# Kernel tuning notes

Hardware: AMD Instinct MI355X
Metric: run time of the kernel (lower is better)

The kernel has to match this reference:

```python
import jax, jax.numpy as jnp
import numpy as np

B, T, C = 4, 2048, 1024
WIN = 16


def setup_inputs() -> dict:
    key = jax.random.key(0)
    ks = jax.random.split(key, 5)
    s = 1.0 / np.sqrt(C)
    return {
        "x": jax.random.normal(ks[0], (B, T, C), dtype=jnp.float32),
        "Wq": jax.random.normal(ks[1], (C, C), dtype=jnp.float32) * s,
        "bq": jnp.zeros((C,), jnp.float32),
        "Wk": jax.random.normal(ks[2], (C, C), dtype=jnp.float32) * s,
        "bk": jnp.zeros((C,), jnp.float32),
        "Wv": jax.random.normal(ks[3], (C, C), dtype=jnp.float32) * s,
        "bv": jnp.zeros((C,), jnp.float32),
        "Wo": jax.random.normal(ks[4], (C, C), dtype=jnp.float32) * s,
        "bo": jnp.zeros((C,), jnp.float32),
        "window": WIN,
    }


def reference(x, Wq, bq, Wk, bk, Wv, bv, Wo, bo, window):
    Bn, Tn, Cn = x.shape
    half = window // 2
    W = 2 * half + 1  # keys per query (window [t-half, t+half])
    q = x @ Wq.T + bq
    k = x @ Wk.T + bk
    v = x @ Wv.T + bv
    offs = jnp.arange(-half, half + 1)              # [W]
    tpos = jnp.arange(Tn)                            # [T]
    idx = tpos[:, None] + offs[None, :]              # [T, W]
    valid = (idx >= 0) & (idx < Tn)                  # [T, W]
    idx_c = jnp.clip(idx, 0, Tn - 1)
    k_win = k[:, idx_c, :]                           # [B, T, W, C]
    v_win = v[:, idx_c, :]                           # [B, T, W, C]
    scale = 1.0 / jnp.sqrt(jnp.asarray(Cn, x.dtype))
    scores = jnp.einsum('btc,btwc->btw', q, k_win) * scale
    scores = jnp.where(valid[None, :, :], scores, jnp.finfo(x.dtype).min)
    attn = jax.nn.softmax(scores, axis=-1)           # [B, T, W]
    ctx = jnp.einsum('btw,btwc->btc', attn, v_win)   # [B, T, C]
    return ctx @ Wo.T + bo
```

## Files before the change

kernel.cpp:

```cpp
#include <hip/hip_runtime.h>
#include <cstdint>
#include <cstddef>

#define B_ 4
#define T_ 2048
#define C_ 1024
#define M_ (B_ * T_)
#define QK_STRIDE 2048
#define NT 32

typedef unsigned short u16;
typedef _Float16 half8 __attribute__((ext_vector_type(8)));
typedef float f32x16 __attribute__((ext_vector_type(16)));
typedef unsigned short ushort8v __attribute__((ext_vector_type(8)));

__device__ __forceinline__ ushort4 cvt4(float4 v) {
    ushort4 o;
    _Float16 a = (_Float16)v.x; o.x = __builtin_bit_cast(unsigned short, a);
    _Float16 b = (_Float16)v.y; o.y = __builtin_bit_cast(unsigned short, b);
    _Float16 c = (_Float16)v.z; o.z = __builtin_bit_cast(unsigned short, c);
    _Float16 d = (_Float16)v.w; o.w = __builtin_bit_cast(unsigned short, d);
    return o;
}


__global__ void prologue2(const float* __restrict__ x,
                          const float* __restrict__ Wq, const float* __restrict__ Wk,
                          const float* __restrict__ Wv, const float* __restrict__ Wo,
                          const float* __restrict__ bq, const float* __restrict__ bk,
                          const float* __restrict__ bv,
                          u16* __restrict__ xf, u16* __restrict__ wfq,
                          u16* __restrict__ wfo, float* __restrict__ bcat) {
    const int blk = blockIdx.x;
    const int tid = threadIdx.x;
    if (blk >= 3072) {
        int i = (blk - 3072) * 256 + tid;
        const float* src = (i < 1024) ? bq : (i < 2048) ? bk : bv;
        bcat[i] = src[i & 1023];
        return;
    }
    __shared__ ushort8v g16[512];
    const float* src;
    u16* dst;
    size_t chunk_base;
    int kg;
    if (blk < 2048) {
        const int mt = blk >> 3; kg = blk & 7;
        src = x + (size_t)mt * 32 * C_;
        dst = xf; chunk_base = (size_t)mt * 64;
    } else {
        const int w = blk - 2048;
        const int mat = w >> 8, nt = (w >> 3) & 31; kg = w & 7;
        src = ((mat == 0) ? Wq : (mat == 1) ? Wk : (mat == 2) ? Wv : Wo)
              + (size_t)nt * 32 * C_;
        if (mat < 3) { dst = wfq; chunk_base = (size_t)(mat * 32 + nt) * 64; }
        else         { dst = wfo; chunk_base = (size_t)nt * 64; }
    }
    const int r = tid >> 3, gc = (tid & 7) * 2;
    const float4* s4 = (const float4*)(src + (size_t)r * C_ + kg * 128 + (tid & 7) * 16);
    float4 f0 = s4[0], f1 = s4[1], f2 = s4[2], f3 = s4[3];
    ushort4 h0 = cvt4(f0), h1 = cvt4(f1), h2 = cvt4(f2), h3 = cvt4(f3);
    ushort8v ga, gb;
    ga[0]=h0.x; ga[1]=h0.y; ga[2]=h0.z; ga[3]=h0.w;
    ga[4]=h1.x; ga[5]=h1.y; ga[6]=h1.z; ga[7]=h1.w;
    gb[0]=h2.x; gb[1]=h2.y; gb[2]=h2.z; gb[3]=h2.w;
    gb[4]=h3.x; gb[5]=h3.y; gb[6]=h3.z; gb[7]=h3.w;
    g16[r * 16 + ((gc    ) ^ (r & 15))] = ga;
    g16[r * 16 + ((gc + 1) ^ (r & 15))] = gb;
    __syncthreads();
    const int lane = tid & 63, rr = lane & 31, hi = lane >> 5;
#pragma unroll
    for (int r2 = 0; r2 < 2; ++r2) {
        const int ksl = r2 * 4 + (tid >> 6);
        const int g = ksl * 2 + hi;
        ushort8v v = g16[rr * 16 + (g ^ (rr & 15))];
        *(ushort8v*)(dst + ((chunk_base + kg * 8 + ksl) * 64 + lane) * 8) = v;
    }
}

#define AS1_ __attribute__((address_space(1)))
#define AS3_ __attribute__((address_space(3)))

__device__ __forceinline__ void gload16(const u16* g, u16* l) {
    __builtin_amdgcn_global_load_lds((AS1_ void*)g, (AS3_ void*)l, 16, 0, 0);
}

#define MFMA_ __builtin_amdgcn_mfma_f32_32x32x16_f16
#define LD8_(p) (*(const half8*)(p))

#define STAGE(NB, KT) { const size_t ko = (size_t)(KT) * 1024;            \
    gload16(gA0 + ko, (NB) + lA0); gload16(gA1 + ko, (NB) + lA1);         \
    gload16(gA2 + ko, (NB) + lA2); gload16(gA3 + ko, (NB) + lA3);         \
    gload16(gB0 + ko, (NB) + lB0); gload16(gB1 + ko, (NB) + lB1); }

#define TILE(CB, NB, KT, DOSTG, VW)                                        \
  {                                                                        \
    half8 a0 = *(const half8*)((CB) + oA);                                 \
    half8 a1 = *(const half8*)((CB) + oA + 1024);                          \
    half8 a2 = *(const half8*)((CB) + oA + 2048);                          \
    half8 a3 = *(const half8*)((CB) + oA + 3072);                          \
    half8 b0v = *(const half8*)((CB) + oB);                                \
    half8 b1v = *(const half8*)((CB) + oB + 1024);                         \
    if (DOSTG) STAGE(NB, (KT) + 2);                                        \
    __builtin_amdgcn_s_setprio(1);                                         \
    acc00 = MFMA_(a0, b0v, acc00, 0, 0, 0);                                \
    acc01 = MFMA_(a0, b1v, acc01, 0, 0, 0);                                \
    acc10 = MFMA_(a1, b0v, acc10, 0, 0, 0);                                \
    acc11 = MFMA_(a1, b1v, acc11, 0, 0, 0);                                \
    acc20 = MFMA_(a2, b0v, acc20, 0, 0, 0);                                \
    acc21 = MFMA_(a2, b1v, acc21, 0, 0, 0);                                \
    acc30 = MFMA_(a3, b0v, acc30, 0, 0, 0);                                \
    acc31 = MFMA_(a3, b1v, acc31, 0, 0, 0);                                \
    __builtin_amdgcn_s_setprio(0);                                         \
    a0 = *(const half8*)((CB) + oA + 512);                                 \
    a1 = *(const half8*)((CB) + oA + 1536);                                \
    a2 = *(const half8*)((CB) + oA + 2560);                                \
    a3 = *(const half8*)((CB) + oA + 3584);                                \
    b0v = *(const half8*)((CB) + oB + 512);                                \
    b1v = *(const half8*)((CB) + oB + 1536);                               \
    __builtin_amdgcn_s_setprio(1);                                         \
    acc00 = MFMA_(a0, b0v, acc00, 0, 0, 0);                                \
    acc01 = MFMA_(a0, b1v, acc01, 0, 0, 0);                                \
    acc10 = MFMA_(a1, b0v, acc10, 0, 0, 0);                                \
    acc11 = MFMA_(a1, b1v, acc11, 0, 0, 0);                                \
    acc20 = MFMA_(a2, b0v, acc20, 0, 0, 0);                                \
    acc21 = MFMA_(a2, b1v, acc21, 0, 0, 0);                                \
    acc30 = MFMA_(a3, b0v, acc30, 0, 0, 0);                                \
    acc31 = MFMA_(a3, b1v, acc31, 0, 0, 0);                                \
    __builtin_amdgcn_s_setprio(0);                                         \
    if ((VW) == 6)      asm volatile("s_waitcnt vmcnt(6) lgkmcnt(0)" ::: "memory"); \
    else if ((VW) == 0) asm volatile("s_waitcnt vmcnt(0) lgkmcnt(0)" ::: "memory"); \
    else                asm volatile("s_waitcnt lgkmcnt(0)" ::: "memory"); \
    asm volatile("s_barrier" ::: "memory");                                \
  }

__global__ __launch_bounds__(256, 2) void gemm_p2(
    const u16* __restrict__ Afrag, const u16* __restrict__ Bfrag,
    const float* __restrict__ bias, u16* __restrict__ qkh,
    u16* __restrict__ vf)
{
    __shared__ u16 lds[3][12288];
    const int tid  = threadIdx.x;
    const int lane = tid & 63;
    const int wave = tid >> 6;
    const int wm   = wave >> 1;
    const int wn   = wave & 1;
    const int la8  = lane * 8;

    const int nb  = gridDim.x * gridDim.y;
    int bid = blockIdx.y * gridDim.x + blockIdx.x;
    bid = (bid & 7) * (nb >> 3) + (bid >> 3);
    const int bx = bid % gridDim.x;
    const int by = bid / gridDim.x;

    const u16* gA0 = Afrag + ((size_t)(by*8 + ((wave    )>>1))*64 + ((wave    )&1))*512 + la8;
    const u16* gA1 = Afrag + ((size_t)(by*8 + ((wave+ 4 )>>1))*64 + ((wave+ 4 )&1))*512 + la8;
    const u16* gA2 = Afrag + ((size_t)(by*8 + ((wave+ 8 )>>1))*64 + ((wave+ 8 )&1))*512 + la8;
    const u16* gA3 = Afrag + ((size_t)(by*8 + ((wave+12 )>>1))*64 + ((wave+12 )&1))*512 + la8;
    const u16* gB0 = Bfrag + ((size_t)(bx*4 + ((wave    )>>1))*64 + ((wave    )&1))*512 + la8;
    const u16* gB1 = Bfrag + ((size_t)(bx*4 + ((wave+ 4 )>>1))*64 + ((wave+ 4 )&1))*512 + la8;
    const int lA0 = (wave     ) * 512;
    const int lA1 = (wave +  4) * 512;
    const int lA2 = (wave +  8) * 512;
    const int lA3 = (wave + 12) * 512;
    const int lB0 = 8192 + (wave    ) * 512;
    const int lB1 = 8192 + (wave + 4) * 512;

    const int oA = wm * 4096 + la8;
    const int oB = 8192 + wn * 2048 + la8;

    u16* b0 = &lds[0][0];
    u16* b1 = &lds[1][0];
    u16* b2 = &lds[2][0];

    STAGE(b0, 0);
    STAGE(b1, 1);
    asm volatile("s_waitcnt vmcnt(6)" ::: "memory");
    asm volatile("s_barrier" ::: "memory");

    f32x16 acc00, acc01, acc10, acc11, acc20, acc21, acc30, acc31;
#pragma unroll
    for (int r = 0; r < 16; ++r) {
        acc00[r] = 0.f; acc01[r] = 0.f; acc10[r] = 0.f; acc11[r] = 0.f;
        acc20[r] = 0.f; acc21[r] = 0.f; acc30[r] = 0.f; acc31[r] = 0.f;
    }

#pragma unroll 1
    for (int kt = 0; kt < NT - 2; kt += 3) {
        TILE(b0, b2, kt,     1, 6);
        TILE(b1, b0, kt + 1, 1, 6);
        TILE(b2, b1, kt + 2, 1, 6);
    }
    TILE(b0, b2, NT - 2, 0, 0);
    TILE(b1, b2, NT - 1, 0, -1);

    const int m0 = by * 256 + wm * 128;
    const int n0 = bx * 128 + wn * 64;
    const int hi = lane >> 5;
    f32x16 accs[4][2] = {{acc00, acc01}, {acc10, acc11}, {acc20, acc21}, {acc30, acc31}};
    if (bx < 16) {
#pragma unroll
        for (int i = 0; i < 4; ++i) {
#pragma unroll
            for (int j = 0; j < 2; ++j) {
                const int col = n0 + j * 32 + (lane & 31);
                const float bv = bias[col];
#pragma unroll
                for (int reg = 0; reg < 16; ++reg) {
                    const int row = m0 + i * 32 + (reg & 3) + 8 * (reg >> 2) + 4 * hi;
                    _Float16 h = (_Float16)(accs[i][j][reg] + bv);
                    qkh[(size_t)row * QK_STRIDE + col] = __builtin_bit_cast(unsigned short, h);
                }
            }
        }
    } else {
#pragma unroll
        for (int i = 0; i < 4; ++i) {
#pragma unroll
            for (int j = 0; j < 2; ++j) {
                const int col = n0 + j * 32 + (lane & 31);
                const int ch  = col - 2048;
                const float bv = bias[col];
#pragma unroll
                for (int rg = 0; rg < 4; ++rg) {
                    ushort4 w;
                    _Float16 h0 = (_Float16)(accs[i][j][4*rg    ] + bv);
                    _Float16 h1 = (_Float16)(accs[i][j][4*rg + 1] + bv);
                    _Float16 h2 = (_Float16)(accs[i][j][4*rg + 2] + bv);
                    _Float16 h3 = (_Float16)(accs[i][j][4*rg + 3] + bv);
                    w.x = __builtin_bit_cast(unsigned short, h0);
                    w.y = __builtin_bit_cast(unsigned short, h1);
                    w.z = __builtin_bit_cast(unsigned short, h2);
                    w.w = __builtin_bit_cast(unsigned short, h3);
                    const size_t chunk = (size_t)((m0 + i * 32 + 8 * rg) >> 4) * 32 + (ch >> 5);
                    const int interior = ((ch & 31) + 32 * (rg & 1)) * 8 + 4 * hi;
                    *(ushort4*)(vf + chunk * 512 + interior) = w;
                }
            }
        }
    }
}

#define STAGE_S0(NB, KO) { gload16(gA0 + (KO), (NB) + lsA0); gload16(gB0 + (KO), (NB) + lsB0); }
#define STAGE_S1(NB, KO) { gload16(gA1 + (KO), (NB) + lsA1); gload16(gB1 + (KO), (NB) + lsB1); }

#define TILE_S(CB, NB, KT, DOSTG, VW)                                      \
  {                                                                        \
    const size_t ko = (size_t)((KT) + 2) * 1024;                           \
    half8 a0 = *(const half8*)((CB) + oA);                                 \
    half8 a1 = *(const half8*)((CB) + oA + 1024);                          \
    half8 b0v = *(const half8*)((CB) + oB);                                \
    half8 b1v = *(const half8*)((CB) + oB + 1024);                         \
    if (DOSTG) STAGE_S0(NB, ko);                                           \
    __builtin_amdgcn_s_setprio(1);                                         \
    acc00 = MFMA_(a0, b0v, acc00, 0, 0, 0);                                \
    acc01 = MFMA_(a0, b1v, acc01, 0, 0, 0);                                \
    acc10 = MFMA_(a1, b0v, acc10, 0, 0, 0);                                \
    acc11 = MFMA_(a1, b1v, acc11, 0, 0, 0);                                \
    __builtin_amdgcn_s_setprio(0);                                         \
    a0 = *(const half8*)((CB) + oA + 512);                                 \
    a1 = *(const half8*)((CB) + oA + 1536);                                \
    b0v = *(const half8*)((CB) + oB + 512);                                \
    b1v = *(const half8*)((CB) + oB + 1536);                               \
    if (DOSTG) STAGE_S1(NB, ko);                                           \
    __builtin_amdgcn_s_setprio(1);                                         \
    acc00 = MFMA_(a0, b0v, acc00, 0, 0, 0);                                \
    acc01 = MFMA_(a0, b1v, acc01, 0, 0, 0);                                \
    acc10 = MFMA_(a1, b0v, acc10, 0, 0, 0);                                \
    acc11 = MFMA_(a1, b1v, acc11, 0, 0, 0);                                \
    __builtin_amdgcn_s_setprio(0);                                         \
    if ((VW) == 4)      asm volatile("s_waitcnt vmcnt(4) lgkmcnt(0)" ::: "memory"); \
    else if ((VW) == 0) asm volatile("s_waitcnt vmcnt(0) lgkmcnt(0)" ::: "memory"); \
    else                asm volatile("s_waitcnt lgkmcnt(0)" ::: "memory"); \
    asm volatile("s_barrier" ::: "memory");                                \
  }

__global__ __launch_bounds__(256, 2) void gemm_s(
    const u16* __restrict__ Afrag, const u16* __restrict__ Bfrag,
    const float* __restrict__ bias, float* __restrict__ Cout, int Ndim)
{
    __shared__ u16 lds[3][8192];
    const int tid  = threadIdx.x;
    const int lane = tid & 63;
    const int wave = tid >> 6;
    const int wm   = wave >> 1;
    const int wn   = wave & 1;
    const int la8  = lane * 8;

    const int nb  = gridDim.x * gridDim.y;
    int bid = blockIdx.y * gridDim.x + blockIdx.x;
    bid = (bid & 7) * (nb >> 3) + (bid >> 3);
    const int bx = bid % gridDim.x;
    const int by = bid / gridDim.x;

    const u16* gA0 = Afrag + ((size_t)(by*4 + ((wave    )>>1))*64 + ((wave    )&1))*512 + la8;
    const u16* gA1 = Afrag + ((size_t)(by*4 + ((wave+ 4 )>>1))*64 + ((wave+ 4 )&1))*512 + la8;
    const u16* gB0 = Bfrag + ((size_t)(bx*4 + ((wave    )>>1))*64 + ((wave    )&1))*512 + la8;
    const u16* gB1 = Bfrag + ((size_t)(bx*4 + ((wave+ 4 )>>1))*64 + ((wave+ 4 )&1))*512 + la8;
    const int lsA0 = (wave    ) * 512;
    const int lsA1 = (wave + 4) * 512;
    const int lsB0 = 4096 + (wave    ) * 512;
    const int lsB1 = 4096 + (wave + 4) * 512;

    const int oA = wm * 2048 + la8;
    const int oB = 4096 + wn * 2048 + la8;

    u16* b0 = &lds[0][0];
    u16* b1 = &lds[1][0];
    u16* b2 = &lds[2][0];

    STAGE_S0(b0, 0); STAGE_S1(b0, 0);
    STAGE_S0(b1, 1024); STAGE_S1(b1, 1024);
    asm volatile("s_waitcnt vmcnt(4)" ::: "memory");
    asm volatile("s_barrier" ::: "memory");

    f32x16 acc00, acc01, acc10, acc11;
#pragma unroll
    for (int r = 0; r < 16; ++r) { acc00[r] = 0.f; acc01[r] = 0.f; acc10[r] = 0.f; acc11[r] = 0.f; }

#pragma unroll 1
    for (int kt = 0; kt < NT - 2; kt += 3) {
        TILE_S(b0, b2, kt,     1, 4);
        TILE_S(b1, b0, kt + 1, 1, 4);
        TILE_S(b2, b1, kt + 2, 1, 4);
    }
    TILE_S(b0, b2, NT - 2, 0, 0);
    TILE_S(b1, b2, NT - 1, 0, -1);

    const int m0 = by * 128 + wm * 64;
    const int n0 = bx * 128 + wn * 64;
    f32x16 accs[2][2] = {{acc00, acc01}, {acc10, acc11}};
#pragma unroll
    for (int i = 0; i < 2; ++i) {
#pragma unroll
        for (int j = 0; j < 2; ++j) {
            const int col = n0 + j * 32 + (lane & 31);
            const float bv = bias[col];
#pragma unroll
            for (int reg = 0; reg < 16; ++reg) {
                const int row = m0 + i * 32 + (reg & 3) + 8 * (reg >> 2) + 4 * (lane >> 5);
                Cout[(size_t)row * Ndim + col] = accs[i][j][reg] + bv;
            }
        }
    }
}

__global__ __launch_bounds__(64) void attn_rm(
    const u16* __restrict__ qkh, const u16* __restrict__ vf,
    u16* __restrict__ ctxf)
{
    const int l   = threadIdx.x;
    const int q   = l & 31;
    const int hi  = l >> 5;
    const int t0  = blockIdx.x * 32;
    const int t0l = t0 & (T_ - 1);

    const int r1 = min(max(t0 - 16 + q, 0), M_ - 1);
    const int r2 = min(max(t0 + 16 + q, 0), M_ - 1);
    const u16* a1p = qkh + (size_t)r1 * QK_STRIDE + 1024 + hi * 8;
    const u16* a2p = qkh + (size_t)r2 * QK_STRIDE + 1024 + hi * 8;
    const u16* qp  = qkh + (size_t)(t0 + q) * QK_STRIDE + hi * 8;

    f32x16 sc1, sc2;
#pragma unroll
    for (int r = 0; r < 16; ++r) { sc1[r] = 0.f; sc2[r] = 0.f; }
#pragma unroll 8
    for (int ks = 0; ks < 64; ++ks) {
        half8 a1 = LD8_(a1p + ks * 16);
        half8 a2 = LD8_(a2p + ks * 16);
        half8 qb = LD8_(qp  + ks * 16);
        sc1 = MFMA_(a1, qb, sc1, 0, 0, 0);
        sc2 = MFMA_(a2, qb, sc2, 0, 0, 0);
    }

    float px1[16], px2[16];
#pragma unroll
    for (int r = 0; r < 16; ++r) {
        px1[r] = __shfl_xor(sc1[r], 32);
        px2[r] = __shfl_xor(sc2[r], 32);
    }

    const int plo = max(q + 8, 16 - t0l);
    const int phi = min(q + 24, (T_ + 15) - t0l);
    float s[64];
#pragma unroll
    for (int p = 0; p < 64; ++p) {
        const int row = p & 31;
        const int h   = (row >> 2) & 1;
        const int rg  = (row & 3) + 4 * (row >> 3);
        const float own = (p < 32) ? sc1[rg] : sc2[rg];
        const float oth = (p < 32) ? px1[rg] : px2[rg];
        const float v = (h == hi) ? own : oth;
        s[p] = (p >= plo && p <= phi) ? v * 0.03125f : -3.0e38f;
    }

    float mx = s[0];
#pragma unroll
    for (int p = 1; p < 64; ++p) mx = fmaxf(mx, s[p]);
    float den = 0.f;
#pragma unroll
    for (int p = 0; p < 64; ++p) { const float w = __expf(s[p] - mx); s[p] = w; den += w; }
    const float inv = 1.f / den;

    half8 pa0, pa1, pa2, pa3;
#pragma unroll
    for (int e = 0; e < 8; ++e) {
        pa0[e] = (_Float16)((hi ? s[ 8 + e] : s[ 0 + e]) * inv);
        pa1[e] = (_Float16)((hi ? s[24 + e] : s[16 + e]) * inv);
        pa2[e] = (_Float16)((hi ? s[40 + e] : s[32 + e]) * inv);
        pa3[e] = (_Float16)((hi ? s[56 + e] : s[48 + e]) * inv);
    }

    const int s0i = (t0 - 16) >> 4;
    const u16* vb0p = vf + (size_t)min(max(s0i    , 0), M_/16 - 1) * 16384 + l * 8;
    const u16* vb1p = vf + (size_t)min(max(s0i + 1, 0), M_/16 - 1) * 16384 + l * 8;
    const u16* vb2p = vf + (size_t)min(max(s0i + 2, 0), M_/16 - 1) * 16384 + l * 8;
    const u16* vb3p = vf + (size_t)min(max(s0i + 3, 0), M_/16 - 1) * 16384 + l * 8;
    const size_t ctxb = (size_t)(t0 >> 5) * 32768;
    const int lpo = 32 * ((l >> 3) & 1);
    const int e7  = l & 7;
#pragma unroll 2
    for (int n = 0; n < 32; ++n) {
        half8 v0 = LD8_(vb0p + n * 512);
        half8 v1 = LD8_(vb1p + n * 512);
        half8 v2 = LD8_(vb2p + n * 512);
        half8 v3 = LD8_(vb3p + n * 512);
        f32x16 o;
#pragma unroll
        for (int r = 0; r < 16; ++r) o[r] = 0.f;
        o = MFMA_(pa0, v0, o, 0, 0, 0);
        o = MFMA_(pa1, v1, o, 0, 0, 0);
        o = MFMA_(pa2, v2, o, 0, 0, 0);
        o = MFMA_(pa3, v3, o, 0, 0, 0);
        u16* cp = ctxf + ctxb + (size_t)(2 * n + (q >> 4)) * 512 + e7;
#pragma unroll
        for (int r = 0; r < 16; ++r) {
            const int mrow = (r & 3) + 8 * (r >> 2) + 4 * hi;
            _Float16 hv = (_Float16)o[r];
            cp[(mrow + lpo) * 8] = __builtin_bit_cast(unsigned short, hv);
        }
    }
}

extern "C" void kernel_launch(void* const* d_in, const int* in_sizes, int n_in,
                              void* d_out, int out_size, void* d_ws, size_t ws_size,
                              hipStream_t stream) {
    const float* x  = (const float*)d_in[0];
    const float* Wq = (const float*)d_in[1];
    const float* bq = (const float*)d_in[2];
    const float* Wk = (const float*)d_in[3];
    const float* bk = (const float*)d_in[4];
    const float* Wv = (const float*)d_in[5];
    const float* bv = (const float*)d_in[6];
    const float* Wo = (const float*)d_in[7];
    const float* bo = (const float*)d_in[8];
    float* out = (float*)d_out;

    const size_t MC = (size_t)M_ * C_;
    u16* xf   = (u16*)d_ws;
    u16* wfq  = xf   + MC;
    u16* wfo  = wfq  + 3 * (size_t)C_ * C_;
    u16* qkh  = wfo  + (size_t)C_ * C_;
    u16* vf   = qkh  + (size_t)M_ * QK_STRIDE;
    u16* ctxf = vf   + MC;
    float* bcat = (float*)(ctxf + MC);

    prologue2<<<3084, 256, 0, stream>>>(x, Wq, Wk, Wv, Wo, bq, bk, bv,
                                        xf, wfq, wfo, bcat);

    dim3 gqkv(3072 / 128, M_ / 256);
    gemm_p2<<<gqkv, 256, 0, stream>>>(xf, wfq, bcat, qkh, vf);

    attn_rm<<<M_ / 32, 64, 0, stream>>>(qkh, vf, ctxf);

    dim3 go(C_ / 128, M_ / 128);
    gemm_s<<<go, 256, 0, stream>>>(ctxf, wfo, bo, out, C_);
}
```

Measured before the change: 228.8 us.

## Replace QKV GEMM with 256x256-tile, 8-wave kernel using 4-stage LDS pipeline

The QKV projection GEMM moves from 256x128 tiles with 4 waves to 256x256 tiles with 8 waves per block. Four waves load A and four load B into a 4-deep LDS ring, and each K tile is split into two k-slices with a barrier between them. The larger tile raises arithmetic intensity per byte loaded and halves redundant A reads. In exchange, occupancy drops to one block per CU, LDS use rises to 128KB, there are more barriers per tile, and the grid shrinks to 384 blocks, which may leave the wave count unbalanced across CUs.

After: 235.4 us. 2.9% more time.

```diff
diff --git a/kernel.cpp b/kernel.cpp
--- a/kernel.cpp
+++ b/kernel.cpp
@@ -87,64 +87,56 @@
 
 #define MFMA_ __builtin_amdgcn_mfma_f32_32x32x16_f16
 #define LD8_(p) (*(const half8*)(p))
-
-#define STAGE(NB, KT) { const size_t ko = (size_t)(KT) * 1024;            \
-    gload16(gA0 + ko, (NB) + lA0); gload16(gA1 + ko, (NB) + lA1);         \
-    gload16(gA2 + ko, (NB) + lA2); gload16(gA3 + ko, (NB) + lA3);         \
-    gload16(gB0 + ko, (NB) + lB0); gload16(gB1 + ko, (NB) + lB1); }
-
-#define TILE(CB, NB, KT, DOSTG, VW)                                        \
-  {                                                                        \
-    half8 a0 = *(const half8*)((CB) + oA);                                 \
-    half8 a1 = *(const half8*)((CB) + oA + 1024);                          \
-    half8 a2 = *(const half8*)((CB) + oA + 2048);                          \
-    half8 a3 = *(const half8*)((CB) + oA + 3072);                          \
-    half8 b0v = *(const half8*)((CB) + oB);                                \
-    half8 b1v = *(const half8*)((CB) + oB + 1024);                         \
-    if (DOSTG) STAGE(NB, (KT) + 2);                                        \
-    __builtin_amdgcn_s_setprio(1);                                         \
-    acc00 = MFMA_(a0, b0v, acc00, 0, 0, 0);                                \
-    acc01 = MFMA_(a0, b1v, acc01, 0, 0, 0);                                \
-    acc10 = MFMA_(a1, b0v, acc10, 0, 0, 0);                                \
-    acc11 = MFMA_(a1, b1v, acc11, 0, 0, 0);                                \
-    acc20 = MFMA_(a2, b0v, acc20, 0, 0, 0);                                \
-    acc21 = MFMA_(a2, b1v, acc21, 0, 0, 0);                                \
-    acc30 = MFMA_(a3, b0v, acc30, 0, 0, 0);                                \
-    acc31 = MFMA_(a3, b1v, acc31, 0, 0, 0);                                \
-    __builtin_amdgcn_s_setprio(0);                                         \
-    a0 = *(const half8*)((CB) + oA + 512);                                 \
-    a1 = *(const half8*)((CB) + oA + 1536);                                \
-    a2 = *(const half8*)((CB) + oA + 2560);                                \
-    a3 = *(const half8*)((CB) + oA + 3584);                                \
-    b0v = *(const half8*)((CB) + oB + 512);                                \
-    b1v = *(const half8*)((CB) + oB + 1536);                               \
-    __builtin_amdgcn_s_setprio(1);                                         \
-    acc00 = MFMA_(a0, b0v, acc00, 0, 0, 0);                                \
-    acc01 = MFMA_(a0, b1v, acc01, 0, 0, 0);                                \
-    acc10 = MFMA_(a1, b0v, acc10, 0, 0, 0);                                \
-    acc11 = MFMA_(a1, b1v, acc11, 0, 0, 0);                                \
-    acc20 = MFMA_(a2, b0v, acc20, 0, 0, 0);                                \
-    acc21 = MFMA_(a2, b1v, acc21, 0, 0, 0);                                \
-    acc30 = MFMA_(a3, b0v, acc30, 0, 0, 0);                                \
-    acc31 = MFMA_(a3, b1v, acc31, 0, 0, 0);                                \
-    __builtin_amdgcn_s_setprio(0);                                         \
-    if ((VW) == 6)      asm volatile("s_waitcnt vmcnt(6) lgkmcnt(0)" ::: "memory"); \
-    else if ((VW) == 0) asm volatile("s_waitcnt vmcnt(0) lgkmcnt(0)" ::: "memory"); \
-    else                asm volatile("s_waitcnt lgkmcnt(0)" ::: "memory"); \
-    asm volatile("s_barrier" ::: "memory");                                \
-  }
-
-__global__ __launch_bounds__(256, 2) void gemm_p2(
+#define BAR_  asm volatile("s_barrier" ::: "memory")
+#define WL0_  asm volatile("s_waitcnt lgkmcnt(0)" ::: "memory")
+
+
+#define WV8_  asm volatile("s_waitcnt vmcnt(8)" ::: "memory")
+#define WV4_  asm volatile("s_waitcnt vmcnt(4)" ::: "memory")
+#define WV0_  asm volatile("s_waitcnt vmcnt(0)" ::: "memory")
+
+#define STG8(SB, HH, RR, S)                                                 \
+    gload16(gw##RR + (size_t)(((HH) + 3) * 2 + (S)) * 512,                  \
+            (SB) + ldst##RR##S)
+
+#define PHASE8(CB, SB, HH, KSL, DOSTG, RR)                                  \
+  { half8 a0 = LD8_((CB) + ((4*wm+0)*2 + (KSL))*512 + la8);                 \
+    half8 a1 = LD8_((CB) + ((4*wm+1)*2 + (KSL))*512 + la8);                 \
+    half8 a2 = LD8_((CB) + ((4*wm+2)*2 + (KSL))*512 + la8);                 \
+    half8 a3 = LD8_((CB) + ((4*wm+3)*2 + (KSL))*512 + la8);                 \
+    half8 bv0 = LD8_((CB) + 8192 + ((2*wn+0)*2 + (KSL))*512 + la8);         \
+    half8 bv1 = LD8_((CB) + 8192 + ((2*wn+1)*2 + (KSL))*512 + la8);         \
+    if (DOSTG) { STG8(SB, HH, RR, 0); STG8(SB, HH, RR, 1); }                \
+    BAR_; WL0_;                                                             \
+    __builtin_amdgcn_s_setprio(1);                                          \
+    acc00 = MFMA_(a0, bv0, acc00, 0, 0, 0);                                 \
+    acc01 = MFMA_(a0, bv1, acc01, 0, 0, 0);                                 \
+    acc10 = MFMA_(a1, bv0, acc10, 0, 0, 0);                                 \
+    acc11 = MFMA_(a1, bv1, acc11, 0, 0, 0);                                 \
+    acc20 = MFMA_(a2, bv0, acc20, 0, 0, 0);                                 \
+    acc21 = MFMA_(a2, bv1, acc21, 0, 0, 0);                                 \
+    acc30 = MFMA_(a3, bv0, acc30, 0, 0, 0);                                 \
+    acc31 = MFMA_(a3, bv1, acc31, 0, 0, 0);                                 \
+    __builtin_amdgcn_s_setprio(0); }
+
+#define HALF8(CB, SB, HH, DOSTG, VW)                                        \
+  { PHASE8(CB, SB, HH, 0, DOSTG, 0); BAR_;                                  \
+    PHASE8(CB, SB, HH, 1, DOSTG, 1);                                        \
+    if ((VW) == 8) { WV8_; } else if ((VW) == 4) { WV4_; }                  \
+    else if ((VW) == 0) { WV0_; }                                           \
+    if ((VW) >= 0) BAR_; }
+
+__global__ __launch_bounds__(512, 1) void gemm8b(
     const u16* __restrict__ Afrag, const u16* __restrict__ Bfrag,
     const float* __restrict__ bias, u16* __restrict__ qkh,
     u16* __restrict__ vf)
 {
-    __shared__ u16 lds[3][12288];
+    __shared__ u16 lds[4][16384];
     const int tid  = threadIdx.x;
     const int lane = tid & 63;
-    const int wave = tid >> 6;
-    const int wm   = wave >> 1;
-    const int wn   = wave & 1;
+    const int w    = tid >> 6;
+    const int wm   = w >> 2;
+    const int wn   = w & 3;
     const int la8  = lane * 8;
 
     const int nb  = gridDim.x * gridDim.y;
@@ -153,30 +145,31 @@
     const int bx = bid % gridDim.x;
     const int by = bid / gridDim.x;
 
-    const u16* gA0 = Afrag + ((size_t)(by*8 + ((wave    )>>1))*64 + ((wave    )&1))*512 + la8;
-    const u16* gA1 = Afrag + ((size_t)(by*8 + ((wave+ 4 )>>1))*64 + ((wave+ 4 )&1))*512 + la8;
-    const u16* gA2 = Afrag + ((size_t)(by*8 + ((wave+ 8 )>>1))*64 + ((wave+ 8 )&1))*512 + la8;
-    const u16* gA3 = Afrag + ((size_t)(by*8 + ((wave+12 )>>1))*64 + ((wave+12 )&1))*512 + la8;
-    const u16* gB0 = Bfrag + ((size_t)(bx*4 + ((wave    )>>1))*64 + ((wave    )&1))*512 + la8;
-    const u16* gB1 = Bfrag + ((size_t)(bx*4 + ((wave+ 4 )>>1))*64 + ((wave+ 4 )&1))*512 + la8;
-    const int lA0 = (wave     ) * 512;
-    const int lA1 = (wave +  4) * 512;
-    const int lA2 = (wave +  8) * 512;
-    const int lA3 = (wave + 12) * 512;
-    const int lB0 = 8192 + (wave    ) * 512;
-    const int lB1 = 8192 + (wave + 4) * 512;
-
-    const int oA = wm * 4096 + la8;
-    const int oB = 8192 + wn * 2048 + la8;
-
-    u16* b0 = &lds[0][0];
-    u16* b1 = &lds[1][0];
-    u16* b2 = &lds[2][0];
-
-    STAGE(b0, 0);
-    STAGE(b1, 1);
-    asm volatile("s_waitcnt vmcnt(6)" ::: "memory");
-    asm volatile("s_barrier" ::: "memory");
+    const int we = w & 3;
+    const u16* gmat = (w < 4) ? Afrag : Bfrag;
+    const int rbase = (w < 4) ? (by * 8 + 2 * we) : (bx * 8 + 2 * we);
+    const int matoff = (w < 4) ? 0 : 8192;
+    const u16* gw0 = gmat + (size_t)(rbase    ) * 64 * 512 + la8;
+    const u16* gw1 = gmat + (size_t)(rbase + 1) * 64 * 512 + la8;
+    const int ldst00 = matoff + ((2 * we    ) * 2 + 0) * 512;
+    const int ldst01 = matoff + ((2 * we    ) * 2 + 1) * 512;
+    const int ldst10 = matoff + ((2 * we + 1) * 2 + 0) * 512;
+    const int ldst11 = matoff + ((2 * we + 1) * 2 + 1) * 512;
+
+    u16* hb0 = &lds[0][0];
+    u16* hb1 = &lds[1][0];
+    u16* hb2 = &lds[2][0];
+    u16* hb3 = &lds[3][0];
+
+#pragma unroll
+    for (int h = 0; h < 3; ++h) {
+        u16* sb = (h == 0) ? hb0 : (h == 1) ? hb1 : hb2;
+        gload16(gw0 + (size_t)(h * 2    ) * 512, sb + ldst00);
+        gload16(gw0 + (size_t)(h * 2 + 1) * 512, sb + ldst01);
+        gload16(gw1 + (size_t)(h * 2    ) * 512, sb + ldst10);
+        gload16(gw1 + (size_t)(h * 2 + 1) * 512, sb + ldst11);
+    }
+    WV8_; BAR_;
 
     f32x16 acc00, acc01, acc10, acc11, acc20, acc21, acc30, acc31;
 #pragma unroll
@@ -186,19 +179,23 @@
     }
 
 #pragma unroll 1
-    for (int kt = 0; kt < NT - 2; kt += 3) {
-        TILE(b0, b2, kt,     1, 6);
-        TILE(b1, b0, kt + 1, 1, 6);
-        TILE(b2, b1, kt + 2, 1, 6);
-    }
-    TILE(b0, b2, NT - 2, 0, 0);
-    TILE(b1, b2, NT - 1, 0, -1);
+    for (int u = 0; u < 7; ++u) {
+        const int H = 4 * u;
+        HALF8(hb0, hb3, H    , 1, 8);
+        HALF8(hb1, hb0, H + 1, 1, 8);
+        HALF8(hb2, hb1, H + 2, 1, 8);
+        HALF8(hb3, hb2, H + 3, 1, 8);
+    }
+    HALF8(hb0, hb3, 28, 1, 8);
+    HALF8(hb1, hb0, 29, 0, 4);
+    HALF8(hb2, hb1, 30, 0, 0);
+    HALF8(hb3, hb2, 31, 0, -1);
 
     const int m0 = by * 256 + wm * 128;
-    const int n0 = bx * 128 + wn * 64;
+    const int n0 = bx * 256 + wn * 64;
     const int hi = lane >> 5;
     f32x16 accs[4][2] = {{acc00, acc01}, {acc10, acc11}, {acc20, acc21}, {acc30, acc31}};
-    if (bx < 16) {
+    if (bx < 8) {
 #pragma unroll
         for (int i = 0; i < 4; ++i) {
 #pragma unroll
@@ -223,18 +220,18 @@
                 const float bv = bias[col];
 #pragma unroll
                 for (int rg = 0; rg < 4; ++rg) {
-                    ushort4 w;
+                    ushort4 wv;
                     _Float16 h0 = (_Float16)(accs[i][j][4*rg    ] + bv);
                     _Float16 h1 = (_Float16)(accs[i][j][4*rg + 1] + bv);
                     _Float16 h2 = (_Float16)(accs[i][j][4*rg + 2] + bv);
                     _Float16 h3 = (_Float16)(accs[i][j][4*rg + 3] + bv);
-                    w.x = __builtin_bit_cast(unsigned short, h0);
-                    w.y = __builtin_bit_cast(unsigned short, h1);
-                    w.z = __builtin_bit_cast(unsigned short, h2);
-                    w.w = __builtin_bit_cast(unsigned short, h3);
+                    wv.x = __builtin_bit_cast(unsigned short, h0);
+                    wv.y = __builtin_bit_cast(unsigned short, h1);
+                    wv.z = __builtin_bit_cast(unsigned short, h2);
+                    wv.w = __builtin_bit_cast(unsigned short, h3);
                     const size_t chunk = (size_t)((m0 + i * 32 + 8 * rg) >> 4) * 32 + (ch >> 5);
                     const int interior = ((ch & 31) + 32 * (rg & 1)) * 8 + 4 * hi;
-                    *(ushort4*)(vf + chunk * 512 + interior) = w;
+                    *(ushort4*)(vf + chunk * 512 + interior) = wv;
                 }
             }
         }
@@ -468,8 +465,8 @@
     prologue2<<<3084, 256, 0, stream>>>(x, Wq, Wk, Wv, Wo, bq, bk, bv,
                                         xf, wfq, wfo, bcat);
 
-    dim3 gqkv(3072 / 128, M_ / 256);
-    gemm_p2<<<gqkv, 256, 0, stream>>>(xf, wfq, bcat, qkh, vf);
+    dim3 gqkv(3072 / 256, M_ / 256);
+    gemm8b<<<gqkv, 512, 0, stream>>>(xf, wfq, bcat, qkh, vf);
 
     attn_rm<<<M_ / 32, 64, 0, stream>>>(qkh, vf, ctxf);
 
```
